# Performance work log

Hardware: AMD Instinct MI355X
Metric: run time of the kernel (lower is better)

## Reference

```python
import jax, jax.numpy as jnp
import numpy as np

DIM = 2048


def setup_inputs() -> dict:
    key = jax.random.key(0)
    k1, k2 = jax.random.split(key)
    skew_kernel = jax.random.normal(k1, (DIM, DIM), dtype=jnp.float32) * 0.01
    dt = jax.random.uniform(k2, (8, 256), dtype=jnp.float32)  # [batch, time]
    return {"skew_kernel": skew_kernel, "dt": dt}


def reference(skew_kernel, dt):
    # Build strictly skew-symmetric A from the upper triangle of the kernel
    K = jnp.triu(skew_kernel, 1)
    A = K - K.T                                  # [dim, dim], A^T = -A
    # H = i*A is Hermitian -> real eigenvalues L_real, unitary V
    H = (1j * A).astype(jnp.complex64)
    L_real, V = jnp.linalg.eigh(H)               # L_real: [dim], V: [dim, dim]
    L = (-1j) * L_real.astype(jnp.complex64)     # purely imaginary spectrum of A
    V_inv = V.conj().T                           # unitary inverse
    # dt broadcasting per original: ndim==2 -> [..., None]; ndim==1 -> [-1,1,1]
    if dt.ndim == 2:
        dt_cast = dt[:, :, None]
    elif dt.ndim == 1:
        dt_cast = dt.reshape(-1, 1, 1)
    else:
        dt_cast = dt[..., None]
    evo_diag = jnp.exp(L[None, None, :] * dt_cast.astype(jnp.complex64))  # [B, T, dim]
    return V, V_inv, evo_diag
```

## Files before the change

### kernel.cpp

```cpp
#include <hip/hip_runtime.h>
#include <math.h>

#define DN 2048
#define LEAF 16
#define NLEAVES 128
#define NB 64
#define SPLITK 32
#define EPSF 5.9604645e-08f
#define SAFMINF 1.17549435e-38f

typedef float2 cplx;

struct Ctl {
  float orgnrm;
  int K;
  int ctot[4];
  float rho;
  int nrot;
  int n12, n23;
};

__device__ __forceinline__ cplx mkc(float x, float y){ cplx c; c.x=x; c.y=y; return c; }
__device__ __forceinline__ cplx cmul(cplx a, cplx b){ return mkc(a.x*b.x - a.y*b.y, a.x*b.y + a.y*b.x); }
__device__ __forceinline__ cplx cconj(cplx a){ return mkc(a.x, -a.y); }
__device__ __forceinline__ cplx cadd(cplx a, cplx b){ return mkc(a.x+b.x, a.y+b.y); }
__device__ __forceinline__ cplx cinv(cplx b){
  if (fabsf(b.x) >= fabsf(b.y)) { float r = b.y/b.x; float den = b.x + b.y*r; return mkc(1.f/den, -r/den); }
  else { float r = b.x/b.y; float den = b.x*r + b.y; return mkc(r/den, -1.f/den); }
}

__global__ void k_buildH(const float* sk, cplx* AH){
  int idx = blockIdx.x*256 + threadIdx.x;
  if (idx >= DN*DN) return;
  int c = idx / DN, r = idx % DN;
  float im;
  if (r > c) im = -sk[(size_t)c*DN + r];
  else if (r < c) im = sk[(size_t)r*DN + c];
  else im = 0.f;
  AH[(size_t)c*DN + r] = mkc(copysignf(0.f, im), im);
}

__global__ void k_clarfg(cplx* AH, cplx* tau, float* e, int j){
  __shared__ float red[256];
  __shared__ cplx ssc; __shared__ int sdo;
  int t = threadIdx.x;
  cplx* col = AH + (size_t)j*DN;
  float ssq = 0.f;
  for (int r = j+2+t; r < DN; r += 256){ cplx v = col[r]; ssq += v.x*v.x + v.y*v.y; }
  red[t]=ssq; __syncthreads();
  for (int s=128;s>0;s>>=1){ if (t<s) red[t]+=red[t+s]; __syncthreads(); }
  if (t==0){
    float xnorm = sqrtf(red[0]);
    cplx alpha = col[j+1];
    if (xnorm == 0.f && alpha.y == 0.f){
      tau[j] = mkc(0.f,0.f); e[j] = alpha.x; sdo = 0;
    } else {
      float beta = -copysignf(sqrtf(alpha.x*alpha.x + alpha.y*alpha.y + xnorm*xnorm), alpha.x);
      tau[j] = mkc((beta - alpha.x)/beta, -alpha.y/beta);
      ssc = cinv(mkc(alpha.x - beta, alpha.y));
      e[j] = beta;
      col[j+1] = mkc(beta, 0.f);
      sdo = 1;
    }
  }
  __syncthreads();
  if (sdo){ cplx sc = ssc; for (int r=j+2+t; r<DN; r+=256) col[r] = cmul(col[r], sc); }
}

__global__ void k_gemv_split(const cplx* AH, cplx* wpart, int j, int m, int chunk){
  int i = blockIdx.x*256 + threadIdx.x;
  int s = blockIdx.y;
  if (i >= m) return;
  int c0 = s*chunk;
  int c1 = c0 + chunk; if (c1 > m) c1 = m;
  const cplx* vcol = AH + (size_t)j*DN + (j+1);
  cplx acc = mkc(0.f,0.f);
  for (int c = c0; c < c1; ++c){
    cplx a = AH[(size_t)(j+1+c)*DN + (j+1+i)];
    cplx v = (c==0)? mkc(1.f,0.f) : vcol[c];
    acc.x += a.x*v.x - a.y*v.y;
    acc.y += a.x*v.y + a.y*v.x;
  }
  wpart[(size_t)s*DN + i] = acc;
}

__global__ void k_axpy(const cplx* AH, const cplx* wpart, cplx* w, const cplx* tau, int j, int m){
  __shared__ float rx[256], ry[256];
  __shared__ cplx salpha;
  int t = threadIdx.x;
  cplx tj = tau[j];
  const cplx* vcol = AH + (size_t)j*DN + (j+1);
  float dx=0.f, dy=0.f;
  for (int i=t; i<m; i+=256){
    cplx acc = mkc(0.f,0.f);
    #pragma unroll
    for (int s=0;s<SPLITK;s++){ cplx p = wpart[(size_t)s*DN + i]; acc.x += p.x; acc.y += p.y; }
    cplx w1 = cmul(tj, acc);
    w[i] = w1;
    cplx v = (i==0)? mkc(1.f,0.f) : vcol[i];
    dx += w1.x*v.x + w1.y*v.y;
    dy += w1.x*v.y - w1.y*v.x;
  }
  rx[t]=dx; ry[t]=dy; __syncthreads();
  for (int s=128;s>0;s>>=1){ if (t<s){ rx[t]+=rx[t+s]; ry[t]+=ry[t+s]; } __syncthreads(); }
  if (t==0){ cplx dot = mkc(rx[0], ry[0]); cplx a = cmul(tj, dot); salpha = mkc(-0.5f*a.x, -0.5f*a.y); }
  __syncthreads();
  cplx al = salpha;
  for (int i=t; i<m; i+=256){ cplx v = (i==0)? mkc(1.f,0.f) : vcol[i]; w[i] = cadd(w[i], cmul(al, v)); }
}

__global__ void k_her2(cplx* AH, const cplx* w, int j, int m){
  int r = blockIdx.x*32 + (threadIdx.x & 31);
  int c = blockIdx.y*8 + (threadIdx.x >> 5);
  if (r >= m || c >= m) return;
  const cplx* vcol = AH + (size_t)j*DN + (j+1);
  cplx vr = (r==0)? mkc(1.f,0.f) : vcol[r];
  cplx vc = (c==0)? mkc(1.f,0.f) : vcol[c];
  cplx wr = w[r], wc = w[c];
  cplx u = cadd(cmul(vr, cconj(wc)), cmul(wr, cconj(vc)));
  size_t idx = (size_t)(j+1+c)*DN + (j+1+r);
  AH[idx].x -= u.x; AH[idx].y -= u.y;
}

__global__ void k_collectD(const cplx* AH, float* d){
  int i = blockIdx.x*256 + threadIdx.x;
  if (i < DN) d[i] = AH[(size_t)i*DN + i].x;
}

__global__ void k_zeroZ(float* Z){
  int idx = blockIdx.x*256 + threadIdx.x;
  if (idx < DN*DN) Z[idx] = 0.f;
}

__global__ void k_predc(float* d, float* e, int* indxq, Ctl* ctl){
  __shared__ float red[256];
  int t = threadIdx.x;
  float mx = 0.f;
  for (int i=t;i<DN;i+=256) mx = fmaxf(mx, fabsf(d[i]));
  for (int i=t;i<DN-1;i+=256) mx = fmaxf(mx, fabsf(e[i]));
  red[t]=mx; __syncthreads();
  for (int s=128;s>0;s>>=1){ if (t<s) red[t]=fmaxf(red[t],red[t+s]); __syncthreads(); }
  float orgnrm = red[0];
  if (t==0) ctl->orgnrm = orgnrm;
  float mul = 1.f/orgnrm;
  __syncthreads();
  for (int i=t;i<DN;i+=256) d[i]*=mul;
  for (int i=t;i<DN-1;i+=256) e[i]*=mul;
  __syncthreads();
  if (t==0){
    for (int b=1;b<NLEAVES;b++){ int s0=b*LEAF; float ae=fabsf(e[s0-1]); d[s0-1]-=ae; d[s0]-=ae; }
  }
  for (int i=t;i<DN;i+=256) indxq[i] = (i & (LEAF-1)) + 1;
}

__device__ void slaev2_d(float a, float b, float c, float* rt1, float* rt2, float* cs1, float* sn1){
  float sm = a + c, df = a - c, adf = fabsf(df), tb = b + b, ab = fabsf(tb);
  float acmx, acmn;
  if (fabsf(a) > fabsf(c)) { acmx = a; acmn = c; } else { acmx = c; acmn = a; }
  float rt;
  if (adf > ab) rt = adf*sqrtf(1.f + (ab/adf)*(ab/adf));
  else if (adf < ab) rt = ab*sqrtf(1.f + (adf/ab)*(adf/ab));
  else rt = ab*sqrtf(2.f);
  int sgn1;
  if (sm < 0.f){ *rt1 = 0.5f*(sm - rt); sgn1 = -1; *rt2 = (acmx/(*rt1))*acmn - (b/(*rt1))*b; }
  else if (sm > 0.f){ *rt1 = 0.5f*(sm + rt); sgn1 = 1; *rt2 = (acmx/(*rt1))*acmn - (b/(*rt1))*b; }
  else { *rt1 = 0.5f*rt; *rt2 = -0.5f*rt; sgn1 = 1; }
  float cs; int sgn2;
  if (df >= 0.f){ cs = df + rt; sgn2 = 1; } else { cs = df - rt; sgn2 = -1; }
  float acs = fabsf(cs);
  if (acs > ab){ float ct = -tb/cs; *sn1 = 1.f/sqrtf(1.f + ct*ct); *cs1 = ct*(*sn1); }
  else {
    if (ab == 0.f){ *cs1 = 1.f; *sn1 = 0.f; }
    else { float tn = -cs/tb; *cs1 = 1.f/sqrtf(1.f + tn*tn); *sn1 = tn*(*cs1); }
  }
  if (sgn1 == sgn2){ float tn = *cs1; *cs1 = -(*sn1); *sn1 = tn; }
}

__device__ void slartg_d(float f, float g, float* cs, float* sn, float* r){
  if (g == 0.f){ *cs = 1.f; *sn = 0.f; *r = f; }
  else if (f == 0.f){ *cs = 0.f; *sn = copysignf(1.f, g); *r = fabsf(g); }
  else {
    float d = sqrtf(f*f + g*g);
    *cs = fabsf(f)/d;
    *r = copysignf(d, f);
    *sn = g/(*r);
  }
}

__device__ void rot1_d(float* z, int ldz, int nr, int col, float cc, float ss){
  for (int r=0;r<nr;++r){
    float tmp = z[(col+1)*ldz + r];
    z[(col+1)*ldz + r] = cc*tmp - ss*z[col*ldz + r];
    z[col*ldz + r] = ss*tmp + cc*z[col*ldz + r];
  }
}

__device__ void ssteqr_small(int n, float* d, float* e, float* z, int ldz){
  for (int c=0;c<n;c++) for (int r=0;r<n;r++) z[c*ldz+r] = (r==c)?1.f:0.f;
  const float eps=EPSF, eps2=eps*eps, safmin=SAFMINF;
  int nmaxit = n*30, jtot=0;
  int l1=0;
  float wc[LEAF], ws_[LEAF];
  while (1){
    if (l1 > n-1) break;
    if (l1 > 0) e[l1-1] = 0.f;
    int m;
    for (m = l1; m <= n-2; ++m){
      float tst = fabsf(e[m]);
      if (tst == 0.f) break;
      if (tst <= (sqrtf(fabsf(d[m]))*sqrtf(fabsf(d[m+1])))*eps){ e[m]=0.f; break; }
    }
    int l = l1, lend = m;
    l1 = m+1;
    if (lend == l) continue;
    if (fabsf(d[lend]) < fabsf(d[l])){ int tmp=l; l=lend; lend=tmp; }
    if (lend > l){
      while (1){
        int mm;
        if (l != lend){
          for (mm = l; mm <= lend-1; ++mm){
            float tst = e[mm]*e[mm];
            if (tst <= (eps2*fabsf(d[mm]))*fabsf(d[mm+1]) + safmin) break;
          }
        } else mm = lend;
        if (mm < lend) e[mm] = 0.f;
        float p = d[l];
        if (mm == l){ d[l]=p; l++; if (l<=lend) continue; else break; }
        if (mm == l+1){
          float rt1, rt2, c_, s_;
          slaev2_d(d[l], e[l], d[l+1], &rt1, &rt2, &c_, &s_);
          rot1_d(z, ldz, n, l, c_, s_);
          d[l]=rt1; d[l+1]=rt2; e[l]=0.f;
          l += 2; if (l<=lend) continue; else break;
        }
        if (jtot == nmaxit) break;
        jtot++;
        float g = (d[l+1]-p)/(2.f*e[l]);
        float rr = sqrtf(g*g+1.f);
        g = d[mm] - p + e[l]/(g + copysignf(rr, g));
        float s_ = 1.f, c_ = 1.f; p = 0.f;
        for (int i = mm-1; i >= l; --i){
          float f = s_*e[i], b = c_*e[i];
          slartg_d(g, f, &c_, &s_, &rr);
          if (i != mm-1) e[i+1] = rr;
          g = d[i+1] - p;
          rr = (d[i]-g)*s_ + 2.f*c_*b;
          p = s_*rr;
          d[i+1] = g+p;
          g = c_*rr - b;
          wc[i] = c_; ws_[i] = -s_;
        }
        for (int q = mm-1; q >= l; --q) rot1_d(z, ldz, n, q, wc[q], ws_[q]);
        d[l] = d[l] - p; e[l] = g;
      }
    } else {
      while (1){
        int mm;
        if (l != lend){
          for (mm = l; mm >= lend+1; --mm){
            float tst = e[mm-1]*e[mm-1];
            if (tst <= (eps2*fabsf(d[mm]))*fabsf(d[mm-1]) + safmin) break;
          }
        } else mm = lend;
        if (mm > lend) e[mm-1] = 0.f;
        float p = d[l];
        if (mm == l){ d[l]=p; l--; if (l>=lend) continue; else break; }
        if (mm == l-1){
          float rt1, rt2, c_, s_;
          slaev2_d(d[l-1], e[l-1], d[l], &rt1, &rt2, &c_, &s_);
          rot1_d(z, ldz, n, l-1, c_, s_);
          d[l-1]=rt1; d[l]=rt2; e[l-1]=0.f;
          l -= 2; if (l>=lend) continue; else break;
        }
        if (jtot == nmaxit) break;
// ... 148 lines not shown
}

__global__ void k_mrot(float* Zmat, const float* rotc, const float* rots,
                       const int* rotp, const int* rotn, const Ctl* ctl, int off, int n){
  int r = blockIdx.x*256 + threadIdx.x;
  if (r >= n) return;
  int nrot = ctl->nrot;
  for (int q=0;q<nrot;++q){
    size_t ip = (size_t)(off+rotp[q])*DN + off + r;
    size_t in_ = (size_t)(off+rotn[q])*DN + off + r;
    float x = Zmat[ip], y = Zmat[in_];
    float cc = rotc[q], ss = rots[q];
    Zmat[ip]  = cc*x + ss*y;
    Zmat[in_] = cc*y - ss*x;
  }
}

__global__ void k_mcopyA(const float* d, const float* Zmat, float* Q2, float* dgrp,
                         const int* indx, const Ctl* ctl, int off, int n, int n1){
  int p = blockIdx.x; if (p >= n) return;
  int t = threadIdx.x; int n2 = n - n1;
  int c0 = ctl->ctot[0], c1 = ctl->ctot[1], c2 = ctl->ctot[2];
  int K = c0+c1+c2;
  int src = indx[p];
  const float* qcol = Zmat + (size_t)(off+src)*DN + off;
  if (t == 0) dgrp[p] = d[off+src];
  size_t base2 = (size_t)n1*(c0+c1);
  size_t base3 = base2 + (size_t)n2*(c1+c2);
  if (p < c0){
    float* dst = Q2 + (size_t)p*n1;
    for (int r=t;r<n1;r+=256) dst[r] = qcol[r];
  } else if (p < c0+c1){
    float* d1 = Q2 + (size_t)p*n1;
    float* d2 = Q2 + base2 + (size_t)(p-c0)*n2;
    for (int r=t;r<n1;r+=256) d1[r] = qcol[r];
    for (int r=t;r<n2;r+=256) d2[r] = qcol[n1+r];
  } else if (p < K){
    float* d2 = Q2 + base2 + (size_t)(p-c0)*n2;
    for (int r=t;r<n2;r+=256) d2[r] = qcol[n1+r];
  } else {
    float* dst = Q2 + base3 + (size_t)(p-K)*n;
    for (int r=t;r<n;r+=256) dst[r] = qcol[r];
  }
}

__global__ void k_mcopyB(float* d, float* Zmat, const float* Q2, const float* dgrp,
                         const Ctl* ctl, int off, int n, int n1){
  int p = blockIdx.x; if (p >= n) return;
  int t = threadIdx.x; int n2 = n - n1;
  int c0 = ctl->ctot[0], c1 = ctl->ctot[1], c2 = ctl->ctot[2];
  int K = c0+c1+c2;
  if (p < K) return;
  size_t base3 = (size_t)n1*(c0+c1) + (size_t)n2*(c1+c2);
  const float* src = Q2 + base3 + (size_t)(p-K)*n;
  float* dst = Zmat + (size_t)(off+p)*DN + off;
  for (int r=t;r<n;r+=256) dst[r] = src[r];
  if (t==0) d[off+p] = dgrp[p];
}

__global__ void k_msec(float* d, float* Zmat, const float* dl, const float* w,
                       const Ctl* ctl, int off){
  int j = blockIdx.x*64 + threadIdx.x;
  int K = ctl->K;
  if (j >= K) return;
  float rho = ctl->rho;
  float* delta = Zmat + (size_t)(off+j)*DN + off;
  if (K == 1){
    d[off] = dl[0] + rho*w[0]*w[0];
    delta[0] = 1.f;
    return;
  }
  int orig; float lo, hi;
  if (j < K-1){
    float gap = dl[j+1] - dl[j];
    float half = 0.5f*gap;
    float fmid = 1.f;
    for (int l=0;l<K;l++){
      float D = (dl[l]-dl[j]) - half;
      fmid += rho*w[l]*w[l]/D;
    }
    if (fmid >= 0.f){ orig = j;   lo = 0.f;   hi = half; }
    else            { orig = j+1; lo = -half; hi = 0.f;  }
  } else {
    float s2 = 0.f;
    for (int l=0;l<K;l++) s2 += w[l]*w[l];
    orig = K-1; lo = 0.f; hi = rho*s2*1.000002f + 1e-30f;
  }
  float dorig = dl[orig];
  float eta = 0.5f*(lo+hi);
  for (int it=0; it<50; ++it){
    float g = 1.f, gp = 0.f;
    for (int l=0;l<K;l++){
      float del = (dl[l]-dorig) - eta;
      float r = w[l]/del;
      g  += rho*w[l]*r;
      gp += rho*r*r;
    }
    if (g > 0.f) hi = eta; else lo = eta;
    float etan = eta - g/gp;
    if (!(etan > lo && etan < hi)) etan = 0.5f*(lo+hi);
    if (etan == eta) break;
    eta = etan;
  }
  d[off+j] = dorig + eta;
  for (int l=0;l<K;l++) delta[l] = (dl[l]-dorig) - eta;
}

__global__ void k_mzhat(const float* dlamda, const float* wkeep, float* what,
                        const float* Zmat, const Ctl* ctl, int off){
  int K = ctl->K;
  int i = blockIdx.x*64 + threadIdx.x;
  if (i >= K) return;
  float acc = Zmat[(size_t)(off+i)*DN + off+i];
  float di = dlamda[i];
  for (int jj=0;jj<K;jj++){
    if (jj==i) continue;
    acc *= Zmat[(size_t)(off+jj)*DN + off+i] / (di - dlamda[jj]);
  }
  what[i] = copysignf(sqrtf(fabsf(acc)), wkeep[i]);
}

__global__ void k_mvec(float* Zmat, const float* what, const int* indxc,
                       const Ctl* ctl, int off){
  __shared__ float sv[2048];
  __shared__ float red[256];
  int K = ctl->K; int j = blockIdx.x;
  if (j >= K) return;
  int t = threadIdx.x;
  float* col = Zmat + (size_t)(off+j)*DN + off;
  float ssq = 0.f;
  for (int i=t;i<K;i+=256){
    float den = col[i];
    if (den == 0.f) den = 1e-30f;
    float v = what[i]/den; sv[i]=v; ssq += v*v;
  }
  red[t]=ssq; __syncthreads();
  for (int s=128;s>0;s>>=1){ if (t<s) red[t]+=red[t+s]; __syncthreads(); }
  float temp = sqrtf(red[0]);
  for (int i=t;i<K;i+=256) col[i] = sv[indxc[i]]/temp;
}

__global__ void k_mcopyS(float* Smat, const float* Zmat, const Ctl* ctl, int off, int mode){
  int K = ctl->K; if (K==0) return;
  int rows = (mode==1)? ctl->n23 : ctl->n12;
  int rowoff = (mode==1)? ctl->ctot[0] : 0;
  if (rows==0) return;
  size_t tot = (size_t)rows*K;
  for (size_t idx = (size_t)blockIdx.x*256+threadIdx.x; idx < tot; idx += (size_t)gridDim.x*256){
    int r = (int)(idx % rows); int c = (int)(idx / rows);
    Smat[idx] = Zmat[(size_t)(off+c)*DN + off + rowoff + r];
  }
}

__global__ void k_sgemm_dc(float* Zmat, const float* Q2, const float* Smat,
                           const Ctl* ctl, int off, int n, int n1, int mode){
  int K = ctl->K; if (K==0) return;
  int n2 = n-n1;
  int m, kk; const float* A; int lda; float* C;
  if (mode==1){ m=n2; kk=ctl->n23; A = Q2 + (size_t)n1*ctl->n12; lda=n2; C = Zmat + (size_t)off*DN + off+n1; }
  else { m=n1; kk=ctl->n12; A = Q2; lda=n1; C = Zmat + (size_t)off*DN + off; }
  const float* B = Smat; int ldb = kk;
  int tr = blockIdx.x*32, tc = blockIdx.y*32;
  if (tr >= m || tc >= K) return;
  __shared__ float As[32][33], Bs[32][33];
  int tx = threadIdx.x & 31, ty = threadIdx.x >> 5;
  float acc[4] = {0.f,0.f,0.f,0.f};
  for (int k0=0;k0<kk;k0+=32){
    for (int q=0;q<4;q++){ int kc=k0+ty+q*8; int r=tr+tx;
      As[tx][ty+q*8] = (r<m && kc<kk)? A[(size_t)kc*lda + r] : 0.f; }
    for (int q=0;q<4;q++){ int cc=tc+ty+q*8; int kr=k0+tx;
      Bs[tx][ty+q*8] = (kr<kk && cc<K)? B[(size_t)cc*ldb + kr] : 0.f; }
    __syncthreads();
    for (int kq=0;kq<32;kq++){
      float a = As[tx][kq];
      #pragma unroll
      for (int q=0;q<4;q++) acc[q] += a*Bs[kq][ty+q*8];
    }
    __syncthreads();
  }
  int r = tr+tx;
  if (r < m){
    for (int q=0;q<4;q++){ int c = tc+ty+q*8; if (c < K) C[(size_t)c*DN + r] = acc[q]; }
  }
}

__global__ void k_mmerge(float* d, int* indxq, const Ctl* ctl, int off, int n){
  int K = ctl->K;
  if (K == 0){ for (int i=0;i<n;i++) indxq[off+i]=i+1; return; }
  int i1=0, i2=n-1, ns1=K, ns2=n-K, k=0;
  while (ns1>0 && ns2>0){
    if (d[off+i1] <= d[off+i2]){ indxq[off+k++]=i1+1; i1++; ns1--; }
    else { indxq[off+k++]=i2+1; i2--; ns2--; }
  }
  while (ns1>0){ indxq[off+k++]=i1+1; i1++; ns1--; }
  while (ns2>0){ indxq[off+k++]=i2+1; i2--; ns2--; }
}

__global__ void k_fpermA(const float* d, const float* Zmat, float* Q2, float* dtmp, const int* indxq){
  int i = blockIdx.x; int t = threadIdx.x;
  int src = indxq[i]-1;
  if (t==0) dtmp[i] = d[src];
  const float* sc = Zmat + (size_t)src*DN;
  float* dc = Q2 + (size_t)i*DN;
  for (int r=t;r<DN;r+=256) dc[r]=sc[r];
}
__global__ void k_fpermB(float* evals, float* Zmat, const float* Q2, const float* dtmp, const Ctl* ctl){
  int i = blockIdx.x; int t = threadIdx.x;
  if (t==0) evals[i] = dtmp[i]*ctl->orgnrm;
  const float* sc = Q2 + (size_t)i*DN;
  float* dc = Zmat + (size_t)i*DN;
  for (int r=t;r<DN;r+=256) dc[r]=sc[r];
}

__global__ void k_packV(const cplx* AH, cplx* Vp, int i0, int ib, int m){
  int idx = blockIdx.x*256 + threadIdx.x;
  if (idx >= m*ib) return;
  int r = idx % m, c = idx / m;
  int grow = i0+1+r, pc = i0+c+1;
  cplx v;
  if (grow < pc) v = mkc(0.f,0.f);
  else if (grow == pc) v = mkc(1.f,0.f);
  else v = AH[(size_t)(i0+c)*DN + grow];
  Vp[(size_t)c*m + r] = v;
}

__global__ void k_vhv(const cplx* Vp, cplx* vhv, int m, int ib){
  __shared__ float rx[256], ry[256];
  int c = blockIdx.x; if (c >= ib) return;
  int t = threadIdx.x;
  for (int r=0; r<c; ++r){
    float dx=0.f, dy=0.f;
    for (int rl=c+t; rl<m; rl+=256){
      cplx a = Vp[(size_t)r*m + rl];
      cplx b = Vp[(size_t)c*m + rl];
      dx += a.x*b.x + a.y*b.y;
      dy += a.x*b.y - a.y*b.x;
    }
    rx[t]=dx; ry[t]=dy; __syncthreads();
    for (int s=128;s>0;s>>=1){ if (t<s){ rx[t]+=rx[t+s]; ry[t]+=ry[t+s]; } __syncthreads(); }
    if (t==0) vhv[r + c*NB] = mkc(rx[0], ry[0]);
    __syncthreads();
  }
}

__global__ void k_bldT(const cplx* vhv, const cplx* tau, cplx* T, int ib){
  int t = threadIdx.x;
  for (int idx=t; idx<NB*NB; idx+=64) T[idx] = mkc(0.f,0.f);
  __syncthreads();
  for (int c=0; c<ib; ++c){
    if (t < c){
      cplx acc = mkc(0.f,0.f);
      for (int q=t; q<c; ++q) acc = cadd(acc, cmul(T[t + q*NB], vhv[q + c*NB]));
      cplx nt = mkc(-tau[c].x, -tau[c].y);
      T[t + c*NB] = cmul(nt, acc);
    }
    if (t == c) T[c + c*NB] = tau[c];
    __syncthreads();
  }
}

__global__ void k_cgemm_ct_p(const cplx* A, const float* Cre, const float* Cim,
                             cplx* G1, int row0, int m, int ib){
  __shared__ cplx As[32][33], Bs[32][33];
  int tr = blockIdx.x*32, tc = blockIdx.y*32;
  if (tr >= ib) return;
  int tx = threadIdx.x & 31, ty = threadIdx.x >> 5;
  cplx acc[4]; for (int q=0;q<4;q++) acc[q]=mkc(0.f,0.f);
  for (int k0=0;k0<m;k0+=32){
    for (int q=0;q<4;q++){ int rr=tr+ty+q*8; int kr=k0+tx;
      As[tx][ty+q*8] = (kr<m && rr<ib)? cconj(A[(size_t)rr*m + kr]) : mkc(0.f,0.f); }
    for (int q=0;q<4;q++){ int cc=tc+ty+q*8; int kr=k0+tx;
      if (kr<m && cc<DN){ size_t bi = (size_t)cc*DN + row0 + kr; Bs[tx][ty+q*8] = mkc(Cre[bi], Cim[bi]); }
      else Bs[tx][ty+q*8] = mkc(0.f,0.f); }
    __syncthreads();
    for (int kq=0;kq<32;kq++){
      cplx a = As[kq][tx];
      #pragma unroll
      for (int q=0;q<4;q++){
        cplx b = Bs[kq][ty+q*8];
        acc[q].x += a.x*b.x - a.y*b.y;
        acc[q].y += a.x*b.y + a.y*b.x;
      }
    }
    __syncthreads();
  }
  int r = tr+tx;
  if (r < ib){
    for (int q=0;q<4;q++){ int c=tc+ty+q*8; if (c<DN) G1[r + (size_t)c*NB] = acc[q]; }
  }
}

__global__ void k_cgemm_nn(const cplx* A, int lda, const cplx* B, int ldb,
                           cplx* C, int ldc, int m, int nn, int kk){
  __shared__ cplx As[32][33], Bs[32][33];
  int tr = blockIdx.x*32, tc = blockIdx.y*32;
  if (tr >= m || tc >= nn) return;
  int tx = threadIdx.x & 31, ty = threadIdx.x >> 5;
  cplx acc[4]; for (int q=0;q<4;q++) acc[q]=mkc(0.f,0.f);
  for (int k0=0;k0<kk;k0+=32){
    for (int q=0;q<4;q++){ int kc=k0+ty+q*8; int r=tr+tx;
      As[tx][ty+q*8] = (r<m && kc<kk)? A[(size_t)kc*lda + r] : mkc(0.f,0.f); }
    for (int q=0;q<4;q++){ int cc=tc+ty+q*8; int kr=k0+tx;
      Bs[tx][ty+q*8] = (kr<kk && cc<nn)? B[(size_t)cc*ldb + kr] : mkc(0.f,0.f); }
    __syncthreads();
    for (int kq=0;kq<32;kq++){
      cplx a = As[tx][kq];
      #pragma unroll
      for (int q=0;q<4;q++){
        cplx b = Bs[kq][ty+q*8];
        acc[q].x += a.x*b.x - a.y*b.y;
        acc[q].y += a.x*b.y + a.y*b.x;
      }
    }
    __syncthreads();
  }
  int r = tr+tx;
  if (r < m){
    for (int q=0;q<4;q++){ int c = tc+ty+q*8; if (c < nn) C[r + (size_t)c*NB] = acc[q]; }
  }
}

__global__ void k_cupdate_p(const cplx* A, const cplx* G2, float* Cre, float* Cim,
                            int row0, int m, int ib){
  __shared__ cplx As[32][33], Bs[32][33];
  int tr = blockIdx.x*32, tc = blockIdx.y*32;
  if (tr >= m) return;
  int tx = threadIdx.x & 31, ty = threadIdx.x >> 5;
  cplx acc[4]; for (int q=0;q<4;q++) acc[q]=mkc(0.f,0.f);
  for (int k0=0;k0<ib;k0+=32){
    for (int q=0;q<4;q++){ int kc=k0+ty+q*8; int r=tr+tx;
      As[tx][ty+q*8] = (r<m && kc<ib)? A[(size_t)kc*m + r] : mkc(0.f,0.f); }
    for (int q=0;q<4;q++){ int cc=tc+ty+q*8; int kr=k0+tx;
      Bs[tx][ty+q*8] = (kr<ib && cc<DN)? G2[kr + (size_t)cc*NB] : mkc(0.f,0.f); }
    __syncthreads();
    for (int kq=0;kq<32;kq++){
      cplx a = As[tx][kq];
      #pragma unroll
      for (int q=0;q<4;q++){
        cplx b = Bs[kq][ty+q*8];
        acc[q].x += a.x*b.x - a.y*b.y;
        acc[q].y += a.x*b.y + a.y*b.x;
      }
    }
    __syncthreads();
  }
  int r = tr+tx;
  if (r < m){
    for (int q=0;q<4;q++){
      int c = tc+ty+q*8;
      if (c < DN){
        size_t idx = (size_t)c*DN + row0 + r;
        Cre[idx] -= acc[q].x;
        Cim[idx] -= acc[q].y;
      }
    }
  }
}

__global__ void k_outVre(const float* Cre, float* out0){
  int idx = blockIdx.x*256 + threadIdx.x;
  if (idx >= DN*DN) return;
  int r = idx >> 11, c = idx & (DN-1);
  out0[idx] = Cre[(size_t)c*DN + r];
}
__global__ void k_outVinv(const float* Cre, float* out1){
  int idx = blockIdx.x*256 + threadIdx.x;
  if (idx >= DN*DN) return;
  out1[idx] = Cre[idx];
}
__global__ void k_outEvo(const float* evals, const float* dt, float* out2, int T){
  int idx = blockIdx.x*256 + threadIdx.x;
  if (idx >= T*DN) return;
  int k = idx & (DN-1), tt = idx >> 11;
  out2[idx] = cosf(evals[k]*dt[tt]);
}

extern "C" void kernel_launch(void* const* d_in, const int* in_sizes, int n_in,
                              void* d_out, int out_size, void* d_ws, size_t ws_size,
                              hipStream_t stream)
{
  const float* sk = (const float*)d_in[0];
  const float* dt = (const float*)d_in[1];
  int Ttot = in_sizes[1];
  float* out = (float*)d_out;
  (void)ws_size; (void)n_in; (void)out_size;

  const size_t N2 = (size_t)DN*DN;
  cplx*  AH   = (cplx*)out;
  float* Smat = out + 2*N2;
  float* Zmat = (float*)d_ws;
  float* Q2   = (float*)d_ws + N2;
  float* Cre  = Zmat;
  float* Cim  = Q2;

  char* wp = (char*)d_ws + 2*N2*sizeof(float);
  auto carve = [&](size_t b)->void*{ void* p=(void*)wp; wp += (b+255)&~(size_t)255; return p; };
  float* dd     = (float*)carve(DN*sizeof(float));
  float* ee     = (float*)carve(DN*sizeof(float));
  float* zz     = (float*)carve(DN*sizeof(float));
  float* dtmp   = (float*)carve(DN*sizeof(float));
  float* dlamda = (float*)carve(DN*sizeof(float));
  float* wkeep  = (float*)carve(DN*sizeof(float));
  float* what   = (float*)carve(DN*sizeof(float));
  float* dgrp   = (float*)carve(DN*sizeof(float));
  float* rotc   = (float*)carve(DN*sizeof(float));
  float* rots   = (float*)carve(DN*sizeof(float));
  float* evals  = (float*)carve(DN*sizeof(float));
  cplx*  tauA   = (cplx*)carve(DN*sizeof(cplx));
  cplx*  wvec   = (cplx*)carve(DN*sizeof(cplx));
  int*   indxq  = (int*)carve(DN*sizeof(int));
  int*   indx   = (int*)carve(DN*sizeof(int));
  int*   indxc  = (int*)carve(DN*sizeof(int));
  int*   indxp  = (int*)carve(DN*sizeof(int));
  int*   coltyp = (int*)carve(DN*sizeof(int));
  int*   rotp   = (int*)carve(DN*sizeof(int));
  int*   rotn   = (int*)carve(DN*sizeof(int));
  Ctl*   ctl    = (Ctl*)carve(sizeof(Ctl));
  cplx*  Vp     = (cplx*)carve((size_t)DN*NB*sizeof(cplx));
  cplx*  G1     = (cplx*)carve((size_t)NB*DN*sizeof(cplx));
  cplx*  G2     = (cplx*)carve((size_t)NB*DN*sizeof(cplx));
  cplx*  Tm     = (cplx*)carve((size_t)NB*NB*sizeof(cplx));
  cplx*  vhv    = (cplx*)carve((size_t)NB*NB*sizeof(cplx));
  cplx*  wpart  = Vp;

  k_buildH<<<(DN*DN+255)/256,256,0,stream>>>(sk, AH);

  for (int j=0; j<=DN-2; ++j){
    int m = DN-1-j;
    k_clarfg<<<1,256,0,stream>>>(AH, tauA, ee, j);
    int chunk = (m + SPLITK - 1)/SPLITK;
    dim3 gv((m+255)/256, SPLITK);
    k_gemv_split<<<gv,256,0,stream>>>(AH, wpart, j, m, chunk);
    k_axpy<<<1,256,0,stream>>>(AH, wpart, wvec, tauA, j, m);
    dim3 g2((m+31)/32,(m+7)/8);
    k_her2<<<g2,256,0,stream>>>(AH, wvec, j, m);
  }
  k_collectD<<<(DN+255)/256,256,0,stream>>>(AH, dd);

  k_zeroZ<<<(DN*DN+255)/256,256,0,stream>>>(Zmat);
  k_predc<<<1,256,0,stream>>>(dd, ee, indxq, ctl);
  k_leaves<<<NLEAVES,64,0,stream>>>(dd, ee, Zmat);

  for (int sz = LEAF; sz < DN; sz *= 2){
    for (int off = 0; off < DN; off += 2*sz){
      int n = 2*sz, n1 = sz;
      k_mprep<<<1,256,0,stream>>>(dd, ee, Zmat, indxq, zz, dtmp, dlamda, wkeep,
                                  indx, indxc, indxp, coltyp, rotc, rots, rotp, rotn,
                                  ctl, off, n, n1);
      k_mrot<<<(n+255)/256,256,0,stream>>>(Zmat, rotc, rots, rotp, rotn, ctl, off, n);
      k_mcopyA<<<n,256,0,stream>>>(dd, Zmat, Q2, dgrp, indx, ctl, off, n, n1);
      k_mcopyB<<<n,256,0,stream>>>(dd, Zmat, Q2, dgrp, ctl, off, n, n1);
      k_msec<<<(n+63)/64,64,0,stream>>>(dd, Zmat, dlamda, wkeep, ctl, off);
      k_mzhat<<<(n+63)/64,64,0,stream>>>(dlamda, wkeep, what, Zmat, ctl, off);
      k_mvec<<<n,256,0,stream>>>(Zmat, what, indxc, ctl, off);
      int gcs = ((n*n)+255)/256; if (gcs > 16384) gcs = 16384;
      k_mcopyS<<<gcs,256,0,stream>>>(Smat, Zmat, ctl, off, 1);
      dim3 gg((n+31)/32,(n+31)/32);
      k_sgemm_dc<<<gg,256,0,stream>>>(Zmat, Q2, Smat, ctl, off, n, n1, 1);
      k_mcopyS<<<gcs,256,0,stream>>>(Smat, Zmat, ctl, off, 2);
      k_sgemm_dc<<<gg,256,0,stream>>>(Zmat, Q2, Smat, ctl, off, n, n1, 2);
      k_mmerge<<<1,1,0,stream>>>(dd, indxq, ctl, off, n);
    }
  }
  k_fpermA<<<DN,256,0,stream>>>(dd, Zmat, Q2, dtmp, indxq);
  k_fpermB<<<DN,256,0,stream>>>(evals, Zmat, Q2, dtmp, ctl);

  k_outEvo<<<((Ttot*DN)+255)/256,256,0,stream>>>(evals, dt, out + 2*N2, Ttot);

  k_zeroZ<<<(DN*DN+255)/256,256,0,stream>>>(Cim);
  int Krefl = DN-1;
  for (int i0 = ((Krefl-1)/NB)*NB; i0 >= 0; i0 -= NB){
    int ib = Krefl - i0; if (ib > NB) ib = NB;
    int m = DN-1-i0;
    int row0 = i0+1;
    k_packV<<<((m*ib)+255)/256,256,0,stream>>>(AH, Vp, i0, ib, m);
    k_vhv<<<ib,256,0,stream>>>(Vp, vhv, m, ib);
    k_bldT<<<1,64,0,stream>>>(vhv, tauA+i0, Tm, ib);
    dim3 gct((ib+31)/32,(DN+31)/32);
    k_cgemm_ct_p<<<gct,256,0,stream>>>(Vp, Cre, Cim, G1, row0, m, ib);
    k_cgemm_nn<<<gct,256,0,stream>>>(Tm, NB, G1, NB, G2, NB, ib, DN, ib);
    dim3 gup((m+31)/32,(DN+31)/32);
    k_cupdate_p<<<gup,256,0,stream>>>(Vp, G2, Cre, Cim, row0, m, ib);
  }

  k_outVre<<<(DN*DN+255)/256,256,0,stream>>>(Cre, out);
  k_outVinv<<<(DN*DN+255)/256,256,0,stream>>>(Cre, out + N2);
}
```

Baseline: 159.4 ms.

## Fuse tridiagonal reduction steps, use 64x64 register tiles, split-K back-transform GEMM

Several independent changes. The Householder step folds clarfg into the split GEMV and a finalize kernel, removing one launch per column, and applies the scaling algebraically after the GEMV. her2 now handles two columns per thread. The divide-and-conquer and back-transform GEMMs move to 64x64 tiles with 4x4 register blocking, and the back-transform GEMM gains a split-K path sized by available workspace. buildH and the output transpose now go through LDS tiles for coalesced access. These target launch overhead and memory bandwidth, at the cost of more registers per thread and an extra split-K reduction.

```diff
diff --git a/kernel.cpp b/kernel.cpp
--- a/kernel.cpp
+++ b/kernel.cpp
@@ -29,97 +29,119 @@
   else { float r = b.x/b.y; float den = b.x*r + b.y; return mkc(r/den, -1.f/den); }
 }
 
-__global__ void k_buildH(const float* sk, cplx* AH){
-  int idx = blockIdx.x*256 + threadIdx.x;
-  if (idx >= DN*DN) return;
-  int c = idx / DN, r = idx % DN;
-  float im;
-  if (r > c) im = -sk[(size_t)c*DN + r];
-  else if (r < c) im = sk[(size_t)r*DN + c];
-  else im = 0.f;
-  AH[(size_t)c*DN + r] = mkc(copysignf(0.f, im), im);
-}
-
-__global__ void k_clarfg(cplx* AH, cplx* tau, float* e, int j){
-  __shared__ float red[256];
-  __shared__ cplx ssc; __shared__ int sdo;
+__global__ void k_buildH_t(const float* sk, cplx* AH){
+  __shared__ float tA[32][33], tB[32][33];
+  int C0 = blockIdx.x*32, R0 = blockIdx.y*32;
+  int tx = threadIdx.x & 31, ty = threadIdx.x >> 5;
+  for (int p=0;p<4;p++){
+    int ry = ty + 8*p;
+    tA[ry][tx] = sk[(size_t)(R0+ry)*DN + C0+tx];
+    tB[ry][tx] = sk[(size_t)(C0+ry)*DN + R0+tx];
+  }
+  __syncthreads();
+  for (int p=0;p<4;p++){
+    int cy = ty + 8*p;
+    int r = R0 + tx, c = C0 + cy;
+    float im;
+    if (r > c) im = -tB[cy][tx];
+    else if (r < c) im = tA[tx][cy];
+    else im = 0.f;
+    AH[(size_t)c*DN + r] = mkc(copysignf(0.f, im), im);
+  }
+}
+
+__global__ void k_gemv_split2(const cplx* AH, cplx* wpart, float* ssqpart, int j, int m, int chunk){
+  int i = blockIdx.x*256 + threadIdx.x;
+  int s = blockIdx.y;
+  int cc0 = s*chunk, cc1 = cc0 + chunk; if (cc1 > m-1) cc1 = m-1;
+  const cplx* x = AH + (size_t)j*DN + (j+2);
+  if (blockIdx.x == 0){
+    __shared__ float red[256];
+    float ss = 0.f;
+    for (int cc = cc0 + threadIdx.x; cc < cc1; cc += 256){ cplx v = x[cc]; ss += v.x*v.x + v.y*v.y; }
+    red[threadIdx.x] = ss; __syncthreads();
+    for (int t=128;t>0;t>>=1){ if (threadIdx.x<t) red[threadIdx.x]+=red[threadIdx.x+t]; __syncthreads(); }
+    if (threadIdx.x == 0) ssqpart[s] = red[0];
+  }
+  if (i >= m) return;
+  cplx acc = mkc(0.f,0.f);
+  for (int cc = cc0; cc < cc1; ++cc){
+    cplx a = AH[(size_t)(j+2+cc)*DN + (j+1+i)];
+    cplx v = x[cc];
+    acc.x += a.x*v.x - a.y*v.y;
+    acc.y += a.x*v.y + a.y*v.x;
+  }
+  wpart[(size_t)s*DN + i] = acc;
+}
+
+__global__ void k_finz(cplx* AH, const cplx* wpart, const float* ssqpart,
+                       cplx* w, cplx* tau, float* e, int j, int m){
+  __shared__ float rx[256], ry[256];
+  __shared__ cplx sssc, stau, salpha;
+  __shared__ int sdo;
   int t = threadIdx.x;
   cplx* col = AH + (size_t)j*DN;
-  float ssq = 0.f;
-  for (int r = j+2+t; r < DN; r += 256){ cplx v = col[r]; ssq += v.x*v.x + v.y*v.y; }
-  red[t]=ssq; __syncthreads();
-  for (int s=128;s>0;s>>=1){ if (t<s) red[t]+=red[t+s]; __syncthreads(); }
-  if (t==0){
-    float xnorm = sqrtf(red[0]);
+  if (t == 0){
+    float xn2 = 0.f;
+    for (int s=0;s<SPLITK;s++) xn2 += ssqpart[s];
+    float xnorm = sqrtf(xn2);
     cplx alpha = col[j+1];
     if (xnorm == 0.f && alpha.y == 0.f){
-      tau[j] = mkc(0.f,0.f); e[j] = alpha.x; sdo = 0;
+      tau[j] = mkc(0.f,0.f); e[j] = alpha.x; sdo = 0; stau = mkc(0.f,0.f); sssc = mkc(0.f,0.f);
     } else {
-      float beta = -copysignf(sqrtf(alpha.x*alpha.x + alpha.y*alpha.y + xnorm*xnorm), alpha.x);
-      tau[j] = mkc((beta - alpha.x)/beta, -alpha.y/beta);
-      ssc = cinv(mkc(alpha.x - beta, alpha.y));
+      float beta = -copysignf(sqrtf(alpha.x*alpha.x + alpha.y*alpha.y + xn2), alpha.x);
+      cplx tj = mkc((beta - alpha.x)/beta, -alpha.y/beta);
+      tau[j] = tj; stau = tj;
+      sssc = cinv(mkc(alpha.x - beta, alpha.y));
       e[j] = beta;
       col[j+1] = mkc(beta, 0.f);
       sdo = 1;
     }
   }
   __syncthreads();
-  if (sdo){ cplx sc = ssc; for (int r=j+2+t; r<DN; r+=256) col[r] = cmul(col[r], sc); }
-}
-
-__global__ void k_gemv_split(const cplx* AH, cplx* wpart, int j, int m, int chunk){
-  int i = blockIdx.x*256 + threadIdx.x;
-  int s = blockIdx.y;
-  if (i >= m) return;
-  int c0 = s*chunk;
-  int c1 = c0 + chunk; if (c1 > m) c1 = m;
-  const cplx* vcol = AH + (size_t)j*DN + (j+1);
-  cplx acc = mkc(0.f,0.f);
-  for (int c = c0; c < c1; ++c){
-    cplx a = AH[(size_t)(j+1+c)*DN + (j+1+i)];
-    cplx v = (c==0)? mkc(1.f,0.f) : vcol[c];
-    acc.x += a.x*v.x - a.y*v.y;
-    acc.y += a.x*v.y + a.y*v.x;
-  }
-  wpart[(size_t)s*DN + i] = acc;
-}
-
-__global__ void k_axpy(const cplx* AH, const cplx* wpart, cplx* w, const cplx* tau, int j, int m){
-  __shared__ float rx[256], ry[256];
-  __shared__ cplx salpha;
-  int t = threadIdx.x;
-  cplx tj = tau[j];
-  const cplx* vcol = AH + (size_t)j*DN + (j+1);
+  cplx ssc = sssc, tj = stau;
+  if (!sdo){
+    for (int i=t;i<m;i+=256) w[i] = mkc(0.f,0.f);
+    return;
+  }
+  for (int r=j+2+t; r<DN; r+=256) col[r] = cmul(col[r], ssc);
+  __syncthreads();
+  const cplx* a0 = AH + (size_t)(j+1)*DN + (j+1);
   float dx=0.f, dy=0.f;
-  for (int i=t; i<m; i+=256){
-    cplx acc = mkc(0.f,0.f);
-    #pragma unroll
-    for (int s=0;s<SPLITK;s++){ cplx p = wpart[(size_t)s*DN + i]; acc.x += p.x; acc.y += p.y; }
-    cplx w1 = cmul(tj, acc);
+  for (int i=t;i<m;i+=256){
+    cplx P = mkc(0.f,0.f);
+    #pragma unroll
+    for (int s=0;s<SPLITK;s++){ cplx p = wpart[(size_t)s*DN + i]; P.x += p.x; P.y += p.y; }
+    cplx av = cadd(a0[i], cmul(ssc, P));
+    cplx w1 = cmul(tj, av);
     w[i] = w1;
-    cplx v = (i==0)? mkc(1.f,0.f) : vcol[i];
+    cplx v = (i==0)? mkc(1.f,0.f) : col[j+1+i];
     dx += w1.x*v.x + w1.y*v.y;
     dy += w1.x*v.y - w1.y*v.x;
   }
   rx[t]=dx; ry[t]=dy; __syncthreads();
   for (int s=128;s>0;s>>=1){ if (t<s){ rx[t]+=rx[t+s]; ry[t]+=ry[t+s]; } __syncthreads(); }
-  if (t==0){ cplx dot = mkc(rx[0], ry[0]); cplx a = cmul(tj, dot); salpha = mkc(-0.5f*a.x, -0.5f*a.y); }
+  if (t==0){ cplx a = cmul(tj, mkc(rx[0], ry[0])); salpha = mkc(-0.5f*a.x, -0.5f*a.y); }
   __syncthreads();
   cplx al = salpha;
-  for (int i=t; i<m; i+=256){ cplx v = (i==0)? mkc(1.f,0.f) : vcol[i]; w[i] = cadd(w[i], cmul(al, v)); }
+  for (int i=t;i<m;i+=256){ cplx v = (i==0)? mkc(1.f,0.f) : col[j+1+i]; w[i] = cadd(w[i], cmul(al, v)); }
 }
 
 __global__ void k_her2(cplx* AH, const cplx* w, int j, int m){
   int r = blockIdx.x*32 + (threadIdx.x & 31);
-  int c = blockIdx.y*8 + (threadIdx.x >> 5);
-  if (r >= m || c >= m) return;
+  int cb = (blockIdx.y*8 + (threadIdx.x >> 5))*2;
+  if (r >= m) return;
   const cplx* vcol = AH + (size_t)j*DN + (j+1);
   cplx vr = (r==0)? mkc(1.f,0.f) : vcol[r];
-  cplx vc = (c==0)? mkc(1.f,0.f) : vcol[c];
-  cplx wr = w[r], wc = w[c];
-  cplx u = cadd(cmul(vr, cconj(wc)), cmul(wr, cconj(vc)));
-  size_t idx = (size_t)(j+1+c)*DN + (j+1+r);
-  AH[idx].x -= u.x; AH[idx].y -= u.y;
+  cplx wr = w[r];
+  for (int c = cb; c < cb+2; ++c){
+    if (c >= m) break;
+    cplx vc = (c==0)? mkc(1.f,0.f) : vcol[c];
+    cplx wc = w[c];
+    cplx u = cadd(cmul(vr, cconj(wc)), cmul(wr, cconj(vc)));
+    size_t idx = (size_t)(j+1+c)*DN + (j+1+r);
+    AH[idx].x -= u.x; AH[idx].y -= u.y;
+  }
 }
 
 __global__ void k_collectD(const cplx* AH, float* d){
@@ -574,36 +596,51 @@
   }
 }
 
-__global__ void k_sgemm_dc(float* Zmat, const float* Q2, const float* Smat,
-                           const Ctl* ctl, int off, int n, int n1, int mode){
+__global__ void k_sgemm_dc64(float* Zmat, const float* Q2, const float* Smat,
+                             const Ctl* ctl, int off, int n, int n1, int mode){
   int K = ctl->K; if (K==0) return;
   int n2 = n-n1;
-  int m, kk; const float* A; int lda; float* C;
-  if (mode==1){ m=n2; kk=ctl->n23; A = Q2 + (size_t)n1*ctl->n12; lda=n2; C = Zmat + (size_t)off*DN + off+n1; }
-  else { m=n1; kk=ctl->n12; A = Q2; lda=n1; C = Zmat + (size_t)off*DN + off; }
-  const float* B = Smat; int ldb = kk;
-  int tr = blockIdx.x*32, tc = blockIdx.y*32;
+  int m, kd; const float* A; int lda; float* C;
+  if (mode==1){ m=n2; kd=ctl->n23; A = Q2 + (size_t)n1*ctl->n12; lda=n2; C = Zmat + (size_t)off*DN + off+n1; }
+  else { m=n1; kd=ctl->n12; A = Q2; lda=n1; C = Zmat + (size_t)off*DN + off; }
+  int tr = blockIdx.x*64, tc = blockIdx.y*64;
   if (tr >= m || tc >= K) return;
-  __shared__ float As[32][33], Bs[32][33];
-  int tx = threadIdx.x & 31, ty = threadIdx.x >> 5;
-  float acc[4] = {0.f,0.f,0.f,0.f};
-  for (int k0=0;k0<kk;k0+=32){
-    for (int q=0;q<4;q++){ int kc=k0+ty+q*8; int r=tr+tx;
-      As[tx][ty+q*8] = (r<m && kc<kk)? A[(size_t)kc*lda + r] : 0.f; }
-    for (int q=0;q<4;q++){ int cc=tc+ty+q*8; int kr=k0+tx;
-      Bs[tx][ty+q*8] = (kr<kk && cc<K)? B[(size_t)cc*ldb + kr] : 0.f; }
+  __shared__ float As[64][17], Bs[16][65];
+  int tid = threadIdx.x, tx = tid & 15, ty = tid >> 4;
+  float acc[4][4];
+  #pragma unroll
+  for (int i=0;i<4;i++) for (int jq=0;jq<4;jq++) acc[i][jq]=0.f;
+  for (int k0=0;k0<kd;k0+=16){
+    #pragma unroll
+    for (int p=0;p<4;p++){
+      int r = tid & 63, kk = (tid >> 6) + 4*p;
+      As[r][kk] = (tr+r<m && k0+kk<kd) ? A[(size_t)(k0+kk)*lda + tr+r] : 0.f;
+    }
+    #pragma unroll
+    for (int p=0;p<4;p++){
+      int kk = tid & 15, c = (tid >> 4) + 16*p;
+      Bs[kk][c] = (k0+kk<kd && tc+c<K) ? Smat[(size_t)(tc+c)*kd + k0+kk] : 0.f;
+    }
     __syncthreads();
-    for (int kq=0;kq<32;kq++){
-      float a = As[tx][kq];
+    #pragma unroll
+    for (int k=0;k<16;k++){
+      float a[4], b[4];
       #pragma unroll
-      for (int q=0;q<4;q++) acc[q] += a*Bs[kq][ty+q*8];
+      for (int i=0;i<4;i++){ a[i]=As[tx+16*i][k]; b[i]=Bs[k][ty+16*i]; }
+      #pragma unroll
+      for (int i=0;i<4;i++)
+        #pragma unroll
+        for (int jq=0;jq<4;jq++) acc[i][jq] += a[i]*b[jq];
     }
     __syncthreads();
   }
-  int r = tr+tx;
-  if (r < m){
-    for (int q=0;q<4;q++){ int c = tc+ty+q*8; if (c < K) C[(size_t)c*DN + r] = acc[q]; }
-  }
+  #pragma unroll
+  for (int i=0;i<4;i++)
+    #pragma unroll
+    for (int jq=0;jq<4;jq++){
+      int r = tr+tx+16*i, c = tc+ty+16*jq;
+      if (r < m && c < K) C[(size_t)c*DN + r] = acc[i][jq];
+    }
 }
 
 __global__ void k_mmerge(float* d, int* indxq, const Ctl* ctl, int off, int n){
@@ -681,39 +718,59 @@
   }
 }
 
-__global__ void k_cgemm_ct_p(const cplx* A, const float* Cre, const float* Cim,
-                             cplx* G1, int row0, int m, int ib){
-  __shared__ cplx As[32][33], Bs[32][33];
-  int tr = blockIdx.x*32, tc = blockIdx.y*32;
-  if (tr >= ib) return;
-  int tx = threadIdx.x & 31, ty = threadIdx.x >> 5;
-  cplx acc[4]; for (int q=0;q<4;q++) acc[q]=mkc(0.f,0.f);
-  for (int k0=0;k0<m;k0+=32){
-    for (int q=0;q<4;q++){ int rr=tr+ty+q*8; int kr=k0+tx;
-      As[tx][ty+q*8] = (kr<m && rr<ib)? cconj(A[(size_t)rr*m + kr]) : mkc(0.f,0.f); }
-    for (int q=0;q<4;q++){ int cc=tc+ty+q*8; int kr=k0+tx;
-      if (kr<m && cc<DN){ size_t bi = (size_t)cc*DN + row0 + kr; Bs[tx][ty+q*8] = mkc(Cre[bi], Cim[bi]); }
-      else Bs[tx][ty+q*8] = mkc(0.f,0.f); }
+__global__ void k_cgemm_ct64(const cplx* A, const float* Cre, const float* Cim,
+                             cplx* G1, int row0, int m, int ib, int ksz){
+  int tc = blockIdx.y*64;
+  int s = blockIdx.z;
+  int ks0 = s*ksz, ks1 = ks0 + ksz; if (ks1 > m) ks1 = m;
+  __shared__ cplx As[64][17], Bs[16][65];
+  int tid = threadIdx.x, tx = tid & 15, ty = tid >> 4;
+  cplx acc[4][4];
+  #pragma unroll
+  for (int i=0;i<4;i++) for (int jq=0;jq<4;jq++) acc[i][jq]=mkc(0.f,0.f);
+  for (int k0 = ks0; k0 < ks1; k0 += 16){
+    #pragma unroll
+    for (int p=0;p<4;p++){
+      int kk = tid & 15, r = (tid >> 4) + 16*p;
+      cplx v = mkc(0.f,0.f);
+      if (r < ib && k0+kk < ks1) v = cconj(A[(size_t)r*m + k0+kk]);
+      As[r][kk] = v;
+    }
+    #pragma unroll
+    for (int p=0;p<4;p++){
+      int kk = tid & 15, c = (tid >> 4) + 16*p;
+      cplx v = mkc(0.f,0.f);
+      int kg = k0+kk, cg = tc+c;
+      if (kg < ks1 && cg < DN){ size_t bi = (size_t)cg*DN + row0 + kg; v = mkc(Cre[bi], Cim[bi]); }
+      Bs[kk][c] = v;
+    }
     __syncthreads();
-    for (int kq=0;kq<32;kq++){
-      cplx a = As[kq][tx];
+    #pragma unroll
+    for (int k=0;k<16;k++){
+      cplx a[4], b[4];
       #pragma unroll
-      for (int q=0;q<4;q++){
-        cplx b = Bs[kq][ty+q*8];
-        acc[q].x += a.x*b.x - a.y*b.y;
-        acc[q].y += a.x*b.y + a.y*b.x;
-      }
+      for (int i=0;i<4;i++){ a[i]=As[tx+16*i][k]; b[i]=Bs[k][ty+16*i]; }
+      #pragma unroll
+      for (int i=0;i<4;i++)
+        #pragma unroll
+        for (int jq=0;jq<4;jq++){
+          acc[i][jq].x += a[i].x*b[jq].x - a[i].y*b[jq].y;
+          acc[i][jq].y += a[i].x*b[jq].y + a[i].y*b[jq].x;
+        }
     }
     __syncthreads();
   }
-  int r = tr+tx;
-  if (r < ib){
-    for (int q=0;q<4;q++){ int c=tc+ty+q*8; if (c<DN) G1[r + (size_t)c*NB] = acc[q]; }
-  }
+  #pragma unroll
+  for (int i=0;i<4;i++)
+    #pragma unroll
+    for (int jq=0;jq<4;jq++){
+      int r = tx+16*i, c = tc+ty+16*jq;
+      if (r < ib && c < DN) G1[(size_t)s*NB*DN + r + (size_t)c*NB] = acc[i][jq];
+    }
 }
 
 __global__ void k_cgemm_nn(const cplx* A, int lda, const cplx* B, int ldb,
-                           cplx* C, int ldc, int m, int nn, int kk){
+                           cplx* C, int ldc, int m, int nn, int kk, int S, int ssz){
   __shared__ cplx As[32][33], Bs[32][33];
   int tr = blockIdx.x*32, tc = blockIdx.y*32;
   if (tr >= m || tc >= nn) return;
@@ -723,7 +780,11 @@
     for (int q=0;q<4;q++){ int kc=k0+ty+q*8; int r=tr+tx;
       As[tx][ty+q*8] = (r<m && kc<kk)? A[(size_t)kc*lda + r] : mkc(0.f,0.f); }
     for (int q=0;q<4;q++){ int cc=tc+ty+q*8; int kr=k0+tx;
-      Bs[tx][ty+q*8] = (kr<kk && cc<nn)? B[(size_t)cc*ldb + kr] : mkc(0.f,0.f); }
+      cplx v = mkc(0.f,0.f);
+      if (kr<kk && cc<nn){
+        for (int s=0;s<S;s++){ cplx u = B[(size_t)s*ssz + kr + (size_t)cc*ldb]; v.x+=u.x; v.y+=u.y; }
+      }
+      Bs[tx][ty+q*8] = v; }
     __syncthreads();
     for (int kq=0;kq<32;kq++){
       cplx a = As[tx][kq];
@@ -742,48 +803,68 @@
   }
 }
 
-__global__ void k_cupdate_p(const cplx* A, const cplx* G2, float* Cre, float* Cim,
+__global__ void k_cupdate64(const cplx* A, const cplx* G2, float* Cre, float* Cim,
                             int row0, int m, int ib){
-  __shared__ cplx As[32][33], Bs[32][33];
-  int tr = blockIdx.x*32, tc = blockIdx.y*32;
+  int tr = blockIdx.x*64, tc = blockIdx.y*64;
   if (tr >= m) return;
+  __shared__ cplx As[64][17], Bs[16][65];
+  int tid = threadIdx.x, tx = tid & 15, ty = tid >> 4;
+  cplx acc[4][4];
+  #pragma unroll
+  for (int i=0;i<4;i++) for (int jq=0;jq<4;jq++) acc[i][jq]=mkc(0.f,0.f);
+  for (int k0=0;k0<ib;k0+=16){
+    #pragma unroll
+    for (int p=0;p<4;p++){
+      int r = tid & 63, kk = (tid >> 6) + 4*p;
+      As[r][kk] = (tr+r<m && k0+kk<ib)? A[(size_t)(k0+kk)*m + tr+r] : mkc(0.f,0.f);
+    }
+    #pragma unroll
+    for (int p=0;p<4;p++){
+      int kk = tid & 15, c = (tid >> 4) + 16*p;
+      Bs[kk][c] = (k0+kk<ib && tc+c<DN)? G2[(k0+kk) + (size_t)(tc+c)*NB] : mkc(0.f,0.f);
+    }
+    __syncthreads();
+    #pragma unroll
+    for (int k=0;k<16;k++){
+      cplx a[4], b[4];
+      #pragma unroll
+      for (int i=0;i<4;i++){ a[i]=As[tx+16*i][k]; b[i]=Bs[k][ty+16*i]; }
+      #pragma unroll
+      for (int i=0;i<4;i++)
+        #pragma unroll
+        for (int jq=0;jq<4;jq++){
+          acc[i][jq].x += a[i].x*b[jq].x - a[i].y*b[jq].y;
+          acc[i][jq].y += a[i].x*b[jq].y + a[i].y*b[jq].x;
+        }
+    }
+    __syncthreads();
+  }
+  #pragma unroll
+  for (int i=0;i<4;i++)
+    #pragma unroll
+    for (int jq=0;jq<4;jq++){
+      int r = tr+tx+16*i, c = tc+ty+16*jq;
+      if (r < m && c < DN){
+        size_t idx = (size_t)c*DN + row0 + r;
+        Cre[idx] -= acc[i][jq].x;
+        Cim[idx] -= acc[i][jq].y;
+      }
+    }
+}
+
+__global__ void k_outVre_t(const float* Cre, float* out0){
+  __shared__ float tile[32][33];
+  int C0 = blockIdx.x*32, R0 = blockIdx.y*32;
   int tx = threadIdx.x & 31, ty = threadIdx.x >> 5;
-  cplx acc[4]; for (int q=0;q<4;q++) acc[q]=mkc(0.f,0.f);
-  for (int k0=0;k0<ib;k0+=32){
-    for (int q=0;q<4;q++){ int kc=k0+ty+q*8; int r=tr+tx;
-      As[tx][ty+q*8] = (r<m && kc<ib)? A[(size_t)kc*m + r] : mkc(0.f,0.f); }
-    for (int q=0;q<4;q++){ int cc=tc+ty+q*8; int kr=k0+tx;
-      Bs[tx][ty+q*8] = (kr<ib && cc<DN)? G2[kr + (size_t)cc*NB] : mkc(0.f,0.f); }
-    __syncthreads();
-    for (int kq=0;kq<32;kq++){
-      cplx a = As[tx][kq];
-      #pragma unroll
-      for (int q=0;q<4;q++){
-        cplx b = Bs[kq][ty+q*8];
-        acc[q].x += a.x*b.x - a.y*b.y;
-        acc[q].y += a.x*b.y + a.y*b.x;
-      }
-    }
-    __syncthreads();
-  }
-  int r = tr+tx;
-  if (r < m){
-    for (int q=0;q<4;q++){
-      int c = tc+ty+q*8;
-      if (c < DN){
-        size_t idx = (size_t)c*DN + row0 + r;
-        Cre[idx] -= acc[q].x;
-        Cim[idx] -= acc[q].y;
-      }
-    }
-  }
-}
-
-__global__ void k_outVre(const float* Cre, float* out0){
-  int idx = blockIdx.x*256 + threadIdx.x;
-  if (idx >= DN*DN) return;
-  int r = idx >> 11, c = idx & (DN-1);
-  out0[idx] = Cre[(size_t)c*DN + r];
+  for (int p=0;p<4;p++){
+    int cy = ty + 8*p;
+    tile[cy][tx] = Cre[(size_t)(C0+cy)*DN + R0+tx];
+  }
+  __syncthreads();
+  for (int p=0;p<4;p++){
+    int ry = ty + 8*p;
+    out0[(size_t)(R0+ry)*DN + C0+tx] = tile[tx][ry];
+  }
 }
 __global__ void k_outVinv(const float* Cre, float* out1){
   int idx = blockIdx.x*256 + threadIdx.x;
@@ -805,7 +886,7 @@
   const float* dt = (const float*)d_in[1];
   int Ttot = in_sizes[1];
   float* out = (float*)d_out;
-  (void)ws_size; (void)n_in; (void)out_size;
+  (void)n_in; (void)out_size;
 
   const size_t N2 = (size_t)DN*DN;
   cplx*  AH   = (cplx*)out;
@@ -828,6 +909,7 @@
   float* rotc   = (float*)carve(DN*sizeof(float));
   float* rots   = (float*)carve(DN*sizeof(float));
   float* evals  = (float*)carve(DN*sizeof(float));
+  float* ssqpart= (float*)carve(64*sizeof(float));
   cplx*  tauA   = (cplx*)carve(DN*sizeof(cplx));
   cplx*  wvec   = (cplx*)carve(DN*sizeof(cplx));
   int*   indxq  = (int*)carve(DN*sizeof(int));
@@ -839,22 +921,28 @@
   int*   rotn   = (int*)carve(DN*sizeof(int));
   Ctl*   ctl    = (Ctl*)carve(sizeof(Ctl));
   cplx*  Vp     = (cplx*)carve((size_t)DN*NB*sizeof(cplx));
-  cplx*  G1     = (cplx*)carve((size_t)NB*DN*sizeof(cplx));
   cplx*  G2     = (cplx*)carve((size_t)NB*DN*sizeof(cplx));
   cplx*  Tm     = (cplx*)carve((size_t)NB*NB*sizeof(cplx));
   cplx*  vhv    = (cplx*)carve((size_t)NB*NB*sizeof(cplx));
+  size_t used = (size_t)(wp - (char*)d_ws);
+  int S = 8;
+  while (S > 1 && (ws_size != 0) && (used + (size_t)S*NB*DN*sizeof(cplx) > ws_size)) S >>= 1;
+  if (ws_size == 0) S = 1;
+  cplx*  G1     = (cplx*)carve((size_t)S*NB*DN*sizeof(cplx));
   cplx*  wpart  = Vp;
 
-  k_buildH<<<(DN*DN+255)/256,256,0,stream>>>(sk, AH);
+  {
+    dim3 gb(DN/32, DN/32);
+    k_buildH_t<<<gb,256,0,stream>>>(sk, AH);
+  }
 
   for (int j=0; j<=DN-2; ++j){
     int m = DN-1-j;
-    k_clarfg<<<1,256,0,stream>>>(AH, tauA, ee, j);
-    int chunk = (m + SPLITK - 1)/SPLITK;
+    int chunk = (m-1 + SPLITK - 1)/SPLITK;
     dim3 gv((m+255)/256, SPLITK);
-    k_gemv_split<<<gv,256,0,stream>>>(AH, wpart, j, m, chunk);
-    k_axpy<<<1,256,0,stream>>>(AH, wpart, wvec, tauA, j, m);
-    dim3 g2((m+31)/32,(m+7)/8);
+    k_gemv_split2<<<gv,256,0,stream>>>(AH, wpart, ssqpart, j, m, chunk);
+    k_finz<<<1,256,0,stream>>>(AH, wpart, ssqpart, wvec, tauA, ee, j, m);
+    dim3 g2((m+31)/32,(m+15)/16);
     k_her2<<<g2,256,0,stream>>>(AH, wvec, j, m);
   }
   k_collectD<<<(DN+255)/256,256,0,stream>>>(AH, dd);
@@ -877,10 +965,10 @@
       k_mvec<<<n,256,0,stream>>>(Zmat, what, indxc, ctl, off);
       int gcs = ((n*n)+255)/256; if (gcs > 16384) gcs = 16384;
       k_mcopyS<<<gcs,256,0,stream>>>(Smat, Zmat, ctl, off, 1);
-      dim3 gg((n+31)/32,(n+31)/32);
-      k_sgemm_dc<<<gg,256,0,stream>>>(Zmat, Q2, Smat, ctl, off, n, n1, 1);
+      dim3 gg((n+63)/64,(n+63)/64);
+      k_sgemm_dc64<<<gg,256,0,stream>>>(Zmat, Q2, Smat, ctl, off, n, n1, 1);
       k_mcopyS<<<gcs,256,0,stream>>>(Smat, Zmat, ctl, off, 2);
-      k_sgemm_dc<<<gg,256,0,stream>>>(Zmat, Q2, Smat, ctl, off, n, n1, 2);
+      k_sgemm_dc64<<<gg,256,0,stream>>>(Zmat, Q2, Smat, ctl, off, n, n1, 2);
       k_mmerge<<<1,1,0,stream>>>(dd, indxq, ctl, off, n);
     }
   }
@@ -898,13 +986,18 @@
     k_packV<<<((m*ib)+255)/256,256,0,stream>>>(AH, Vp, i0, ib, m);
     k_vhv<<<ib,256,0,stream>>>(Vp, vhv, m, ib);
     k_bldT<<<1,64,0,stream>>>(vhv, tauA+i0, Tm, ib);
-    dim3 gct((ib+31)/32,(DN+31)/32);
-    k_cgemm_ct_p<<<gct,256,0,stream>>>(Vp, Cre, Cim, G1, row0, m, ib);
-    k_cgemm_nn<<<gct,256,0,stream>>>(Tm, NB, G1, NB, G2, NB, ib, DN, ib);
-    dim3 gup((m+31)/32,(DN+31)/32);
-    k_cupdate_p<<<gup,256,0,stream>>>(Vp, G2, Cre, Cim, row0, m, ib);
-  }
-
-  k_outVre<<<(DN*DN+255)/256,256,0,stream>>>(Cre, out);
+    int ksz = ((m + S - 1)/S + 15) & ~15;
+    dim3 gct(1, DN/64, S);
+    k_cgemm_ct64<<<gct,256,0,stream>>>(Vp, Cre, Cim, G1, row0, m, ib, ksz);
+    dim3 gnn((ib+31)/32, (DN+31)/32);
+    k_cgemm_nn<<<gnn,256,0,stream>>>(Tm, NB, G1, NB, G2, NB, ib, DN, ib, S, NB*DN);
+    dim3 gup((m+63)/64, DN/64);
+    k_cupdate64<<<gup,256,0,stream>>>(Vp, G2, Cre, Cim, row0, m, ib);
+  }
+
+  {
+    dim3 gt(DN/32, DN/32);
+    k_outVre_t<<<gt,256,0,stream>>>(Cre, out);
+  }
   k_outVinv<<<(DN*DN+255)/256,256,0,stream>>>(Cre, out + N2);
 }
```

After: 164.7 ms. +3.3%, slower.
